# Performance work log

Hardware: AMD Instinct MI355X
Metric: run time of the kernel (lower is better)

## Reference

```python
import jax, jax.numpy as jnp
import numpy as np
import math

H = 8
E = 512
D_K = E // H
NEG = -1000000000.0
# last (and only surviving) row of dist_bar: one threshold per head
DIST_BAR = np.array([0.2, 0.3, 0.4, 0.5, 0.6, 0.7, 0.8, 0.9], dtype=np.float32)


def setup_inputs() -> dict:
    key = jax.random.key(0)
    ks = jax.random.split(key, 12)
    B, N = 8, 1024
    s = 1.0 / math.sqrt(E)
    inp = {
        "query": jax.random.normal(ks[0], (B, N, E), jnp.float32),
        "key": jax.random.normal(ks[1], (B, N, E), jnp.float32),
        "value": jax.random.normal(ks[2], (B, N, E), jnp.float32),
        "dist": jax.random.uniform(ks[3], (B, 1, N, N), jnp.float32),
        "mask": jnp.ones((B, N, N), jnp.int32),
        "Wq": jax.random.normal(ks[4], (E, E), jnp.float32) * s,
        "bq": jnp.zeros((E,), jnp.float32),
        "Wk": jax.random.normal(ks[5], (E, E), jnp.float32) * s,
        "bk": jnp.zeros((E,), jnp.float32),
        "Wv": jax.random.normal(ks[6], (E, E), jnp.float32) * s,
        "bv": jnp.zeros((E,), jnp.float32),
        "Wo": jax.random.normal(ks[7], (E, E), jnp.float32) * s,
        "bo": jnp.zeros((E,), jnp.float32),
    }
    return inp


def reference(query, key, value, dist, mask, Wq, bq, Wk, bk, Wv, bv, Wo, bo):
    B, N, _ = query.shape
    # project and split heads: [B, H, N, D_K]
    def heads(x, W, b):
        return (x @ W.T + b).reshape(B, N, H, D_K).transpose(0, 2, 1, 3)
    q = heads(query, Wq, bq)
    k = heads(key, Wk, bk)
    v = heads(value, Wv, bv)
    scores = jnp.einsum("bhqd,bhkd->bhqk", q, k) / math.sqrt(D_K)
    # padding mask: [B,N,N] -> [B,1,N,N]
    scores = jnp.where(mask[:, None, :, :] == 0, NEG, scores)
    # per-head distance mask: dist [B,1,N,N] < thr[h] -> [B,H,N,N]
    thr = jnp.asarray(DIST_BAR)[None, :, None, None]
    dmask = dist < thr
    # first row/col (global atom) always attend
    dmask = dmask.at[:, :, 0, :].set(True).at[:, :, :, 0].set(True)
    scores = jnp.where(dmask, scores, NEG)
    p = jax.nn.softmax(scores, axis=-1)
    out = jnp.einsum("bhqk,bhkd->bhqd", p, v)  # [B,H,N,D_K]
    out = out.transpose(0, 2, 1, 3).reshape(B, N, H * D_K)
    return out @ Wo.T + bo
```

## Files before the change

### kernel.cpp

```cpp
#include <hip/hip_runtime.h>
#include <stdint.h>


typedef __attribute__((ext_vector_type(8))) short short8;
typedef __attribute__((ext_vector_type(4))) float floatx4;

#define MFMA16(a, b, c) __builtin_amdgcn_mfma_f32_16x16x32_bf16((a), (b), (c), 0, 0, 0)
#define QSCALE 0.1803368801111362f

static __device__ __forceinline__ unsigned short f2bf(float f) {
  union { float f; unsigned u; } v; v.f = f;
  unsigned r = v.u + 0x7fffu + ((v.u >> 16) & 1u);
  return (unsigned short)(r >> 16);
}

static __device__ __forceinline__ void gload_lds16(const void* g, void* l) {
  __builtin_amdgcn_global_load_lds((const __attribute__((address_space(1))) unsigned int*)g,
                                   (__attribute__((address_space(3))) unsigned int*)l,
                                   16, 0, 0);
}
static __device__ __forceinline__ int xsw(int row) { return (row & 3) ^ ((row >> 2) & 3); }

__global__ void cast_all(const float* __restrict__ q, const float* __restrict__ k,
                         const float* __restrict__ v,
                         const float* __restrict__ wq, const float* __restrict__ wk,
                         const float* __restrict__ wv, const float* __restrict__ wo,
                         unsigned short* __restrict__ qb, unsigned short* __restrict__ kb,
                         unsigned short* __restrict__ vb,
                         unsigned short* __restrict__ wq16, unsigned short* __restrict__ wk16,
                         unsigned short* __restrict__ wv16, unsigned short* __restrict__ wo16) {
  int i = blockIdx.x * blockDim.x + threadIdx.x;
  const float* s; unsigned short* d; int loc;
  if (i < 3145728) {
    int w = i >> 20; loc = i & 1048575;
    s = (w == 0) ? q : (w == 1) ? k : v;
    d = (w == 0) ? qb : (w == 1) ? kb : vb;
  } else {
    int j = i - 3145728; int w = j >> 16; loc = j & 65535;
    s = (w == 0) ? wq : (w == 1) ? wk : (w == 2) ? wv : wo;
    d = (w == 0) ? wq16 : (w == 1) ? wk16 : (w == 2) ? wv16 : wo16;
  }
  float4 vv = ((const float4*)s)[loc];
  ushort4 o;
  o.x = f2bf(vv.x); o.y = f2bf(vv.y); o.z = f2bf(vv.z); o.w = f2bf(vv.w);
  ((ushort4*)d)[loc] = o;
}

__global__ void codes_kernel(const float* __restrict__ dist, const int* __restrict__ mask,
                             unsigned char* __restrict__ codesP) {
  int t = blockIdx.x * blockDim.x + threadIdx.x;
  int flat = t << 2;
  int b = flat >> 20;
  int rem = flat & ((1 << 20) - 1);
  int row = rem >> 10;
  int col0 = rem & 1023;
  float4 d4 = ((const float4*)dist)[t];
  int4 m4 = ((const int4*)mask)[t];
  float dv[4] = {d4.x, d4.y, d4.z, d4.w};
  int mv[4] = {m4.x, m4.y, m4.z, m4.w};
  int rg = row >> 5;
  int st = (row >> 4) & 1;
  int qq = (row >> 2) & 3;
  int r = row & 3;
  size_t rowbase = (size_t)(b * 32 + rg) * 32768;
  int sub = st * 32 + r;
#pragma unroll
  for (int u = 0; u < 4; u++) {
    int col = col0 + u;
    float d = dv[u];
    int hmin = (d >= 0.2f) + (d >= 0.3f) + (d >= 0.4f) + (d >= 0.5f) +
               (d >= 0.6f) + (d >= 0.7f) + (d >= 0.8f) + (d >= 0.9f);
    unsigned char cc = (unsigned char)hmin;
    if (row == 0 || col == 0) cc = 0;
    if (mv[u] == 0) cc = 9;
    int kt = col >> 7, ci = (col >> 4) & 7, c = col & 15;
    int lane = qq * 16 + c;
    codesP[rowbase + (size_t)kt * 4096 + lane * 64 + sub + ci * 4] = cc;
  }
}

__global__ __launch_bounds__(256) void qkv_gemm(
    const unsigned short* __restrict__ Aq, const unsigned short* __restrict__ Ak,
    const unsigned short* __restrict__ Av,
    const unsigned short* __restrict__ Wqp, const unsigned short* __restrict__ Wkp,
    const unsigned short* __restrict__ Wvp,
    const float* __restrict__ bq, const float* __restrict__ bk, const float* __restrict__ bv,
    unsigned short* __restrict__ Qh, unsigned short* __restrict__ Kh,
    unsigned short* __restrict__ Vt) {
  const int z = blockIdx.z;
  const unsigned short* A = (z == 0) ? Aq : (z == 1) ? Ak : Av;
  const unsigned short* W = (z == 0) ? Wqp : (z == 1) ? Wkp : Wvp;
  const float* bias = (z == 0) ? bq : (z == 1) ? bk : bv;
  unsigned short* O = (z == 0) ? Qh : (z == 1) ? Kh : Vt;

  __shared__ __align__(16) short As[128 * 32];
  __shared__ __align__(16) short Bs[128 * 32];
  const int tid = threadIdx.x;
  const int lane = tid & 63;
  const int wave = tid >> 6;
  const int c = lane & 15;
  const int q = lane >> 4;
  const int m0 = blockIdx.x * 128;
  const int n0 = blockIdx.y * 128;
  const int wr = (wave >> 1) * 64;
  const int wc = (wave & 1) * 64;

  floatx4 acc[4][4];
#pragma unroll
  for (int i = 0; i < 4; i++)
#pragma unroll
    for (int j = 0; j < 4; j++) acc[i][j] = (floatx4)(0.0f);

  for (int k0 = 0; k0 < 512; k0 += 32) {
    __syncthreads();
#pragma unroll
    for (int it = 0; it < 2; it++) {
      int slot = wave * 128 + it * 64 + lane;
      int row = slot >> 2, ch = slot & 3;
      int g = ch ^ xsw(row);
      gload_lds16(A + (size_t)(m0 + row) * 512 + k0 + g * 8, &As[(wave * 128 + it * 64) * 8]);
      gload_lds16(W + (size_t)(n0 + row) * 512 + k0 + g * 8, &Bs[(wave * 128 + it * 64) * 8]);
    }
    __syncthreads();

    short8 af[4], bfv[4];
#pragma unroll
    for (int i = 0; i < 4; i++) {
      int row = wr + i * 16 + c;
      af[i] = *(const short8*)(&As[row * 32 + (q ^ xsw(row)) * 8]);
    }
#pragma unroll
    for (int j = 0; j < 4; j++) {
      int row = wc + j * 16 + c;
      bfv[j] = *(const short8*)(&Bs[row * 32 + (q ^ xsw(row)) * 8]);
    }
#pragma unroll
    for (int i = 0; i < 4; i++)
#pragma unroll
      for (int j = 0; j < 4; j++)
        acc[i][j] = MFMA16(af[i], bfv[j], acc[i][j]);
  }

  const float scale = (z == 0) ? QSCALE : 1.0f;
#pragma unroll
  for (int i = 0; i < 4; i++) {
    int gm0 = m0 + wr + i * 16 + q * 4;
#pragma unroll
    for (int j = 0; j < 4; j++) {
      int gn = n0 + wc + j * 16 + c;
      float bb = bias[gn];
      int h = gn >> 6, d = gn & 63;
      if (z == 2) {
        int b = gm0 >> 10, n = gm0 & 1023;
        ushort4 pk;
#pragma unroll
        for (int r = 0; r < 4; r++) pk[r] = f2bf(acc[i][j][r] + bb);
        *(ushort4*)(&Vt[(((size_t)(b * 8 + h) * 64 + d) << 10) + n]) = pk;
      } else {
#pragma unroll
        for (int r = 0; r < 4; r++) {
          int m = gm0 + r;
          int b = m >> 10, n = m & 1023;
          O[((((size_t)(b * 8 + h)) << 10) + n) * 64 + d] = f2bf((acc[i][j][r] + bb) * scale);
        }
      }
    }
  }
}

__global__ __launch_bounds__(256) void out_gemm(const unsigned short* __restrict__ A,
                                                const unsigned short* __restrict__ W,
                                                const float* __restrict__ bias,
                                                float* __restrict__ Out) {
  __shared__ __align__(16) short As[128 * 32];
  __shared__ __align__(16) short Bs[64 * 32];
  const int tid = threadIdx.x;
  const int lane = tid & 63;
  const int wave = tid >> 6;
  const int c = lane & 15;
  const int q = lane >> 4;
  const int m0 = blockIdx.x * 128;
  const int n0 = blockIdx.y * 64;
  const int wr = (wave >> 1) * 64;
  const int wc = (wave & 1) * 32;

  floatx4 acc[4][2];
#pragma unroll
  for (int i = 0; i < 4; i++)
#pragma unroll
    for (int j = 0; j < 2; j++) acc[i][j] = (floatx4)(0.0f);

  for (int k0 = 0; k0 < 512; k0 += 32) {
    __syncthreads();
#pragma unroll
    for (int it = 0; it < 2; it++) {
      int slot = wave * 128 + it * 64 + lane;
      int row = slot >> 2, ch = slot & 3;
      int g = ch ^ xsw(row);
      gload_lds16(A + (size_t)(m0 + row) * 512 + k0 + g * 8, &As[(wave * 128 + it * 64) * 8]);
    }
    {
      int slot = wave * 64 + lane;
      int row = slot >> 2, ch = slot & 3;
      int g = ch ^ xsw(row);
      gload_lds16(W + (size_t)(n0 + row) * 512 + k0 + g * 8, &Bs[(wave * 64) * 8]);
    }
    __syncthreads();

    short8 af[4], bfv[2];
#pragma unroll
    for (int i = 0; i < 4; i++) {
      int row = wr + i * 16 + c;
      af[i] = *(const short8*)(&As[row * 32 + (q ^ xsw(row)) * 8]);
    }
#pragma unroll
    for (int j = 0; j < 2; j++) {
      int row = wc + j * 16 + c;
      bfv[j] = *(const short8*)(&Bs[row * 32 + (q ^ xsw(row)) * 8]);
    }
#pragma unroll
    for (int i = 0; i < 4; i++)
#pragma unroll
      for (int j = 0; j < 2; j++)
        acc[i][j] = MFMA16(af[i], bfv[j], acc[i][j]);
  }

#pragma unroll
  for (int i = 0; i < 4; i++) {
    int gm0 = m0 + wr + i * 16 + q * 4;
#pragma unroll
    for (int j = 0; j < 2; j++) {
      int gn = n0 + wc + j * 16 + c;
      float bb = bias[gn];
#pragma unroll
      for (int r = 0; r < 4; r++)
        Out[(size_t)(gm0 + r) * 512 + gn] = acc[i][j][r] + bb;
    }
  }
}

__global__ __launch_bounds__(256) void attn_kernel(const unsigned short* __restrict__ Qh,
                                                   const unsigned short* __restrict__ Kh,
                                                   const unsigned short* __restrict__ Vt,
                                                   const unsigned char* __restrict__ codesP,
                                                   unsigned short* __restrict__ AO) {
  __shared__ __align__(16) unsigned short P[4][16 * 132];
  const int tid = threadIdx.x;
  const int lane = tid & 63;
  const int wave = tid >> 6;
  const int c = lane & 15;
  const int q = lane >> 4;
  const int bh = blockIdx.y;
  const int b = bh >> 3;
  const int h = bh & 7;
  const size_t base = (size_t)bh << 16;
  const int rbase = blockIdx.x * 64 + wave * 16;
  const int rg = rbase >> 5;
  const int st = (rbase >> 4) & 1;
  unsigned short* Pw = &P[wave][0];

  short8 aq[2];
#pragma unroll
  for (int kk = 0; kk < 2; kk++)
    aq[kk] = *(const short8*)(Qh + base + (size_t)(rbase + c) * 64 + kk * 32 + q * 8);

  const unsigned char* cbt = codesP + (size_t)(b * 32 + rg) * 32768 + lane * 64 + st * 32;
  const unsigned short* Kb = Kh + base;
  const unsigned short* Vb = Vt + base;

  float rs[4] = {0.0f, 0.0f, 0.0f, 0.0f};
  floatx4 o[4];
#pragma unroll
  for (int ci = 0; ci < 4; ci++) o[ci] = (floatx4)(0.0f);

  for (int kt = 0; kt < 8; kt++) {
    const unsigned short* Kt = Kb + (size_t)kt * 128 * 64;
    floatx4 s[8];
#pragma unroll
    for (int ci = 0; ci < 8; ci++) s[ci] = (floatx4)(0.0f);
#pragma unroll
    for (int ci = 0; ci < 8; ci++)
#pragma unroll
      for (int kk = 0; kk < 2; kk++) {
        short8 bk = *(const short8*)(Kt + (size_t)(ci * 16 + c) * 64 + kk * 32 + q * 8);
        s[ci] = MFMA16(aq[kk], bk, s[ci]);
      }
    const unsigned char* cp = cbt + (size_t)kt * 4096;
    uint4 w0 = *(const uint4*)(cp);
    uint4 w1 = *(const uint4*)(cp + 16);
    unsigned cv[8] = {w0.x, w0.y, w0.z, w0.w, w1.x, w1.y, w1.z, w1.w};
#pragma unroll
    for (int ci = 0; ci < 8; ci++)
#pragma unroll
      for (int r = 0; r < 4; r++) {
        int code = (cv[ci] >> (r * 8)) & 0xff;
        float e = (h >= code) ? exp2f(s[ci][r]) : 0.0f;
        rs[r] += e;
        Pw[(q * 4 + r) * 132 + ci * 16 + c] = f2bf(e);
      }
#pragma unroll
    for (int ch = 0; ch < 4; ch++) {
      short8 ap = *(const short8*)(&Pw[(size_t)c * 132 + ch * 32 + q * 8]);
#pragma unroll
      for (int ci = 0; ci < 4; ci++) {
        short8 bv = *(const short8*)(Vb + (size_t)(ci * 16 + c) * 1024 + kt * 128 + ch * 32 + q * 8);
        o[ci] = MFMA16(ap, bv, o[ci]);
      }
    }
  }

  float inv[4];
#pragma unroll
  for (int r = 0; r < 4; r++) {
    float v = rs[r];
    v += __shfl_xor(v, 1); v += __shfl_xor(v, 2);
    v += __shfl_xor(v, 4); v += __shfl_xor(v, 8);
    inv[r] = 1.0f / v;
  }
#pragma unroll
  for (int r = 0; r < 4; r++) {
    int n = rbase + q * 4 + r;
    size_t ob = ((size_t)((b << 10) + n)) * 512 + h * 64;
#pragma unroll
    for (int ci = 0; ci < 4; ci++)
      AO[ob + ci * 16 + c] = f2bf(o[ci][r] * inv[r]);
  }
}

extern "C" void kernel_launch(void* const* d_in, const int* in_sizes, int n_in,
                              void* d_out, int out_size, void* d_ws, size_t ws_size,
                              hipStream_t stream) {
  const float* query = (const float*)d_in[0];
  const float* key_  = (const float*)d_in[1];
  const float* value = (const float*)d_in[2];
  const float* dist  = (const float*)d_in[3];
  const int*   mask  = (const int*)d_in[4];
  const float* Wq = (const float*)d_in[5];
  const float* bq = (const float*)d_in[6];
  const float* Wk = (const float*)d_in[7];
  const float* bk = (const float*)d_in[8];
  const float* Wv = (const float*)d_in[9];
  const float* bv = (const float*)d_in[10];
  const float* Wo = (const float*)d_in[11];
  const float* bo = (const float*)d_in[12];

  char* ws = (char*)d_ws;
  size_t off = 0;
  auto alloc = [&](size_t bytes) -> char* {
    char* p = ws + off;
    off += (bytes + 255) & ~(size_t)255;
    return p;
  };
  const size_t NQKV = 8192ull * 512;
  unsigned short* qb   = (unsigned short*)alloc(NQKV * 2);
  unsigned short* kb   = (unsigned short*)alloc(NQKV * 2);
  unsigned short* vb   = (unsigned short*)alloc(NQKV * 2);
  unsigned short* wq16 = (unsigned short*)alloc(512ull * 512 * 2);
  unsigned short* wk16 = (unsigned short*)alloc(512ull * 512 * 2);
  unsigned short* wv16 = (unsigned short*)alloc(512ull * 512 * 2);
  unsigned short* wo16 = (unsigned short*)alloc(512ull * 512 * 2);
  unsigned short* Qh = (unsigned short*)alloc(NQKV * 2);
  unsigned short* Kh = (unsigned short*)alloc(NQKV * 2);
  unsigned short* Vt = (unsigned short*)alloc(NQKV * 2);
  unsigned short* AO = (unsigned short*)alloc(NQKV * 2);
  unsigned char*  codesP = (unsigned char*)alloc(8ull * 1024 * 1024);

  cast_all<<<13312, 256, 0, stream>>>(query, key_, value, Wq, Wk, Wv, Wo,
                                      qb, kb, vb, wq16, wk16, wv16, wo16);
  codes_kernel<<<8192, 256, 0, stream>>>(dist, mask, codesP);
  qkv_gemm<<<dim3(64, 4, 3), 256, 0, stream>>>(qb, kb, vb, wq16, wk16, wv16,
                                               bq, bk, bv, Qh, Kh, Vt);
  attn_kernel<<<dim3(16, 64), 256, 0, stream>>>(Qh, Kh, Vt, codesP, AO);
  out_gemm<<<dim3(64, 8), 256, 0, stream>>>(AO, wo16, bo, (float*)d_out);
}
```

Before: 332.8 us.

## Split KV across wave pairs in attention, merge prep kernels, vectorize QK stores

The attention kernel now has each wave handle 32 query rows (two 16-row subtiles) over half of the key range. This reuses each K and V fragment load for two MFMAs, and partial outputs and row sums are combined through LDS after a block barrier. The cast and codes kernels are merged into one launch. The Q/K projection epilogue swaps operand roles so results can be written as packed ushort4 stores instead of scalar ones. In exchange, register pressure, LDS use and an extra synchronization step go up.

```diff
diff --git a/kernel.cpp b/kernel.cpp
--- a/kernel.cpp
+++ b/kernel.cpp
@@ -21,80 +21,82 @@
 }
 static __device__ __forceinline__ int xsw(int row) { return (row & 3) ^ ((row >> 2) & 3); }
 
-__global__ void cast_all(const float* __restrict__ q, const float* __restrict__ k,
-                         const float* __restrict__ v,
-                         const float* __restrict__ wq, const float* __restrict__ wk,
-                         const float* __restrict__ wv, const float* __restrict__ wo,
-                         unsigned short* __restrict__ qb, unsigned short* __restrict__ kb,
-                         unsigned short* __restrict__ vb,
-                         unsigned short* __restrict__ wq16, unsigned short* __restrict__ wk16,
-                         unsigned short* __restrict__ wv16, unsigned short* __restrict__ wo16) {
-  int i = blockIdx.x * blockDim.x + threadIdx.x;
-  const float* s; unsigned short* d; int loc;
-  if (i < 3145728) {
-    int w = i >> 20; loc = i & 1048575;
-    s = (w == 0) ? q : (w == 1) ? k : v;
-    d = (w == 0) ? qb : (w == 1) ? kb : vb;
+__global__ void prep_kernel(const float* __restrict__ q, const float* __restrict__ k,
+                            const float* __restrict__ v,
+                            const float* __restrict__ wq, const float* __restrict__ wk,
+                            const float* __restrict__ wv, const float* __restrict__ wo,
+                            const float* __restrict__ dist, const int* __restrict__ mask,
+                            unsigned short* __restrict__ qb, unsigned short* __restrict__ kb,
+                            unsigned short* __restrict__ vb,
+                            unsigned short* __restrict__ wq16, unsigned short* __restrict__ wk16,
+                            unsigned short* __restrict__ wv16, unsigned short* __restrict__ wo16,
+                            unsigned char* __restrict__ codesP) {
+  int gb = blockIdx.x;
+  if (gb < 13312) {
+    int i = gb * 256 + threadIdx.x;
+    const float* s; unsigned short* d; int loc;
+    if (i < 3145728) {
+      int w = i >> 20; loc = i & 1048575;
+      s = (w == 0) ? q : (w == 1) ? k : v;
+      d = (w == 0) ? qb : (w == 1) ? kb : vb;
+    } else {
+      int j = i - 3145728; int w = j >> 16; loc = j & 65535;
+      s = (w == 0) ? wq : (w == 1) ? wk : (w == 2) ? wv : wo;
+      d = (w == 0) ? wq16 : (w == 1) ? wk16 : (w == 2) ? wv16 : wo16;
+    }
+    float4 vv = ((const float4*)s)[loc];
+    ushort4 o;
+    o.x = f2bf(vv.x); o.y = f2bf(vv.y); o.z = f2bf(vv.z); o.w = f2bf(vv.w);
+    ((ushort4*)d)[loc] = o;
   } else {
-    int j = i - 3145728; int w = j >> 16; loc = j & 65535;
-    s = (w == 0) ? wq : (w == 1) ? wk : (w == 2) ? wv : wo;
-    d = (w == 0) ? wq16 : (w == 1) ? wk16 : (w == 2) ? wv16 : wo16;
-  }
-  float4 vv = ((const float4*)s)[loc];
-  ushort4 o;
-  o.x = f2bf(vv.x); o.y = f2bf(vv.y); o.z = f2bf(vv.z); o.w = f2bf(vv.w);
-  ((ushort4*)d)[loc] = o;
-}
-
-__global__ void codes_kernel(const float* __restrict__ dist, const int* __restrict__ mask,
-                             unsigned char* __restrict__ codesP) {
-  int t = blockIdx.x * blockDim.x + threadIdx.x;
-  int flat = t << 2;
-  int b = flat >> 20;
-  int rem = flat & ((1 << 20) - 1);
-  int row = rem >> 10;
-  int col0 = rem & 1023;
-  float4 d4 = ((const float4*)dist)[t];
-  int4 m4 = ((const int4*)mask)[t];
-  float dv[4] = {d4.x, d4.y, d4.z, d4.w};
-  int mv[4] = {m4.x, m4.y, m4.z, m4.w};
-  int rg = row >> 5;
-  int st = (row >> 4) & 1;
-  int qq = (row >> 2) & 3;
-  int r = row & 3;
-  size_t rowbase = (size_t)(b * 32 + rg) * 32768;
-  int sub = st * 32 + r;
-#pragma unroll
-  for (int u = 0; u < 4; u++) {
-    int col = col0 + u;
-    float d = dv[u];
-    int hmin = (d >= 0.2f) + (d >= 0.3f) + (d >= 0.4f) + (d >= 0.5f) +
-               (d >= 0.6f) + (d >= 0.7f) + (d >= 0.8f) + (d >= 0.9f);
-    unsigned char cc = (unsigned char)hmin;
-    if (row == 0 || col == 0) cc = 0;
-    if (mv[u] == 0) cc = 9;
-    int kt = col >> 7, ci = (col >> 4) & 7, c = col & 15;
-    int lane = qq * 16 + c;
-    codesP[rowbase + (size_t)kt * 4096 + lane * 64 + sub + ci * 4] = cc;
+    int t = (gb - 13312) * 256 + threadIdx.x;
+    int flat = t << 2;
+    int b = flat >> 20;
+    int rem = flat & ((1 << 20) - 1);
+    int row = rem >> 10;
+    int col0 = rem & 1023;
+    float4 d4 = ((const float4*)dist)[t];
+    int4 m4 = ((const int4*)mask)[t];
+    float dv[4] = {d4.x, d4.y, d4.z, d4.w};
+    int mv[4] = {m4.x, m4.y, m4.z, m4.w};
+    int rg = row >> 5;
+    int st = (row >> 4) & 1;
+    int qq = (row >> 2) & 3;
+    int r = row & 3;
+    size_t rowbase = (size_t)(b * 32 + rg) * 32768;
+    int sub = st * 32 + r;
+#pragma unroll
+    for (int u = 0; u < 4; u++) {
+      int col = col0 + u;
+      float d = dv[u];
+      int hmin = (d >= 0.2f) + (d >= 0.3f) + (d >= 0.4f) + (d >= 0.5f) +
+                 (d >= 0.6f) + (d >= 0.7f) + (d >= 0.8f) + (d >= 0.9f);
+      unsigned char cc = (unsigned char)hmin;
+      if (row == 0 || col == 0) cc = 0;
+      if (mv[u] == 0) cc = 9;
+      int kt = col >> 7, ci = (col >> 4) & 7, c = col & 15;
+      int lane = qq * 16 + c;
+      codesP[rowbase + (size_t)kt * 4096 + lane * 64 + sub + ci * 4] = cc;
+    }
   }
 }
 
 __global__ __launch_bounds__(256) void qkv_gemm(
-    const unsigned short* __restrict__ Aq, const unsigned short* __restrict__ Ak,
-    const unsigned short* __restrict__ Av,
+    const unsigned short* __restrict__ Xq, const unsigned short* __restrict__ Xk,
+    const unsigned short* __restrict__ Xv,
     const unsigned short* __restrict__ Wqp, const unsigned short* __restrict__ Wkp,
     const unsigned short* __restrict__ Wvp,
     const float* __restrict__ bq, const float* __restrict__ bk, const float* __restrict__ bv,
     unsigned short* __restrict__ Qh, unsigned short* __restrict__ Kh,
     unsigned short* __restrict__ Vt) {
   const int z = blockIdx.z;
-  const unsigned short* A = (z == 0) ? Aq : (z == 1) ? Ak : Av;
+  const unsigned short* X = (z == 0) ? Xq : (z == 1) ? Xk : Xv;
   const unsigned short* W = (z == 0) ? Wqp : (z == 1) ? Wkp : Wvp;
   const float* bias = (z == 0) ? bq : (z == 1) ? bk : bv;
   unsigned short* O = (z == 0) ? Qh : (z == 1) ? Kh : Vt;
 
-  __shared__ __align__(16) short As[128 * 32];
-  __shared__ __align__(16) short Bs[128 * 32];
+  __shared__ __align__(16) short Xs[128 * 32];
+  __shared__ __align__(16) short Ws[128 * 32];
   const int tid = threadIdx.x;
   const int lane = tid & 63;
   const int wave = tid >> 6;
@@ -118,21 +120,23 @@
       int slot = wave * 128 + it * 64 + lane;
       int row = slot >> 2, ch = slot & 3;
       int g = ch ^ xsw(row);
-      gload_lds16(A + (size_t)(m0 + row) * 512 + k0 + g * 8, &As[(wave * 128 + it * 64) * 8]);
-      gload_lds16(W + (size_t)(n0 + row) * 512 + k0 + g * 8, &Bs[(wave * 128 + it * 64) * 8]);
+      gload_lds16(X + (size_t)(m0 + row) * 512 + k0 + g * 8, &Xs[(wave * 128 + it * 64) * 8]);
+      gload_lds16(W + (size_t)(n0 + row) * 512 + k0 + g * 8, &Ws[(wave * 128 + it * 64) * 8]);
     }
     __syncthreads();
 
+    const short* Pa = (z == 2) ? Xs : Ws;
+    const short* Pb = (z == 2) ? Ws : Xs;
     short8 af[4], bfv[4];
 #pragma unroll
     for (int i = 0; i < 4; i++) {
       int row = wr + i * 16 + c;
-      af[i] = *(const short8*)(&As[row * 32 + (q ^ xsw(row)) * 8]);
+      af[i] = *(const short8*)(&Pa[row * 32 + (q ^ xsw(row)) * 8]);
     }
 #pragma unroll
     for (int j = 0; j < 4; j++) {
       int row = wc + j * 16 + c;
-      bfv[j] = *(const short8*)(&Bs[row * 32 + (q ^ xsw(row)) * 8]);
+      bfv[j] = *(const short8*)(&Pb[row * 32 + (q ^ xsw(row)) * 8]);
     }
 #pragma unroll
     for (int i = 0; i < 4; i++)
@@ -141,28 +145,38 @@
         acc[i][j] = MFMA16(af[i], bfv[j], acc[i][j]);
   }
 
-  const float scale = (z == 0) ? QSCALE : 1.0f;
-#pragma unroll
-  for (int i = 0; i < 4; i++) {
-    int gm0 = m0 + wr + i * 16 + q * 4;
-#pragma unroll
-    for (int j = 0; j < 4; j++) {
-      int gn = n0 + wc + j * 16 + c;
-      float bb = bias[gn];
-      int h = gn >> 6, d = gn & 63;
-      if (z == 2) {
-        int b = gm0 >> 10, n = gm0 & 1023;
+  if (z == 2) {
+#pragma unroll
+    for (int i = 0; i < 4; i++) {
+      int gm0 = m0 + wr + i * 16 + q * 4;
+      int b = gm0 >> 10, n = gm0 & 1023;
+#pragma unroll
+      for (int j = 0; j < 4; j++) {
+        int gn = n0 + wc + j * 16 + c;
+        float bb = bias[gn];
+        int h = gn >> 6, d = gn & 63;
         ushort4 pk;
 #pragma unroll
         for (int r = 0; r < 4; r++) pk[r] = f2bf(acc[i][j][r] + bb);
         *(ushort4*)(&Vt[(((size_t)(b * 8 + h) * 64 + d) << 10) + n]) = pk;
-      } else {
-#pragma unroll
-        for (int r = 0; r < 4; r++) {
-          int m = gm0 + r;
-          int b = m >> 10, n = m & 1023;
-          O[((((size_t)(b * 8 + h)) << 10) + n) * 64 + d] = f2bf((acc[i][j][r] + bb) * scale);
-        }
+      }
+    }
+  } else {
+    const float scale = (z == 0) ? QSCALE : 1.0f;
+#pragma unroll
+    for (int i = 0; i < 4; i++) {
+      int f0 = n0 + wr + i * 16 + q * 4;
+      float4 bb4 = *(const float4*)(bias + f0);
+      int h = f0 >> 6, d0 = f0 & 63;
+      float bbs[4] = {bb4.x, bb4.y, bb4.z, bb4.w};
+#pragma unroll
+      for (int j = 0; j < 4; j++) {
+        int t = m0 + wc + j * 16 + c;
+        int b = t >> 10, n = t & 1023;
+        ushort4 pk;
+#pragma unroll
+        for (int r = 0; r < 4; r++) pk[r] = f2bf((acc[i][j][r] + bbs[r]) * scale);
+        *(ushort4*)(&O[((((size_t)(b * 8 + h)) << 10) + n) * 64 + d0]) = pk;
       }
     }
   }
@@ -239,12 +253,13 @@
   }
 }
 
-__global__ __launch_bounds__(256) void attn_kernel(const unsigned short* __restrict__ Qh,
-                                                   const unsigned short* __restrict__ Kh,
-                                                   const unsigned short* __restrict__ Vt,
-                                                   const unsigned char* __restrict__ codesP,
-                                                   unsigned short* __restrict__ AO) {
-  __shared__ __align__(16) unsigned short P[4][16 * 132];
+__global__ __launch_bounds__(256, 4) void attn_kernel(const unsigned short* __restrict__ Qh,
+                                                      const unsigned short* __restrict__ Kh,
+                                                      const unsigned short* __restrict__ Vt,
+                                                      const unsigned char* __restrict__ codesP,
+                                                      unsigned short* __restrict__ AO) {
+  __shared__ __align__(16) unsigned short P[4][32 * 132];
+  __shared__ float rsx[2][32];
   const int tid = threadIdx.x;
   const int lane = tid & 63;
   const int wave = tid >> 6;
@@ -254,76 +269,126 @@
   const int b = bh >> 3;
   const int h = bh & 7;
   const size_t base = (size_t)bh << 16;
-  const int rbase = blockIdx.x * 64 + wave * 16;
+  const int qc = wave >> 1;
+  const int kvh = wave & 1;
+  const int rbase = blockIdx.x * 64 + qc * 32;
   const int rg = rbase >> 5;
-  const int st = (rbase >> 4) & 1;
   unsigned short* Pw = &P[wave][0];
 
-  short8 aq[2];
-#pragma unroll
-  for (int kk = 0; kk < 2; kk++)
-    aq[kk] = *(const short8*)(Qh + base + (size_t)(rbase + c) * 64 + kk * 32 + q * 8);
-
-  const unsigned char* cbt = codesP + (size_t)(b * 32 + rg) * 32768 + lane * 64 + st * 32;
+  short8 aq[2][2];
+#pragma unroll
+  for (int st = 0; st < 2; st++)
+#pragma unroll
+    for (int kk = 0; kk < 2; kk++)
+      aq[st][kk] = *(const short8*)(Qh + base + (size_t)(rbase + st * 16 + c) * 64 + kk * 32 + q * 8);
+
+  const unsigned char* cbt = codesP + (size_t)(b * 32 + rg) * 32768 + lane * 64;
   const unsigned short* Kb = Kh + base;
   const unsigned short* Vb = Vt + base;
 
-  float rs[4] = {0.0f, 0.0f, 0.0f, 0.0f};
-  floatx4 o[4];
-#pragma unroll
-  for (int ci = 0; ci < 4; ci++) o[ci] = (floatx4)(0.0f);
-
-  for (int kt = 0; kt < 8; kt++) {
+  float rs[2][4];
+#pragma unroll
+  for (int st = 0; st < 2; st++)
+#pragma unroll
+    for (int r = 0; r < 4; r++) rs[st][r] = 0.0f;
+  floatx4 o[2][4];
+#pragma unroll
+  for (int st = 0; st < 2; st++)
+#pragma unroll
+    for (int ci = 0; ci < 4; ci++) o[st][ci] = (floatx4)(0.0f);
+
+  for (int kt = kvh * 4; kt < kvh * 4 + 4; kt++) {
     const unsigned short* Kt = Kb + (size_t)kt * 128 * 64;
-    floatx4 s[8];
-#pragma unroll
-    for (int ci = 0; ci < 8; ci++) s[ci] = (floatx4)(0.0f);
+    floatx4 s[2][8];
+#pragma unroll
+    for (int ci = 0; ci < 8; ci++) { s[0][ci] = (floatx4)(0.0f); s[1][ci] = (floatx4)(0.0f); }
 #pragma unroll
     for (int ci = 0; ci < 8; ci++)
 #pragma unroll
       for (int kk = 0; kk < 2; kk++) {
         short8 bk = *(const short8*)(Kt + (size_t)(ci * 16 + c) * 64 + kk * 32 + q * 8);
-        s[ci] = MFMA16(aq[kk], bk, s[ci]);
+        s[0][ci] = MFMA16(aq[0][kk], bk, s[0][ci]);
+        s[1][ci] = MFMA16(aq[1][kk], bk, s[1][ci]);
       }
     const unsigned char* cp = cbt + (size_t)kt * 4096;
     uint4 w0 = *(const uint4*)(cp);
     uint4 w1 = *(const uint4*)(cp + 16);
-    unsigned cv[8] = {w0.x, w0.y, w0.z, w0.w, w1.x, w1.y, w1.z, w1.w};
-#pragma unroll
-    for (int ci = 0; ci < 8; ci++)
-#pragma unroll
-      for (int r = 0; r < 4; r++) {
-        int code = (cv[ci] >> (r * 8)) & 0xff;
-        float e = (h >= code) ? exp2f(s[ci][r]) : 0.0f;
-        rs[r] += e;
-        Pw[(q * 4 + r) * 132 + ci * 16 + c] = f2bf(e);
-      }
+    uint4 w2 = *(const uint4*)(cp + 32);
+    uint4 w3 = *(const uint4*)(cp + 48);
+    unsigned cv[16] = {w0.x, w0.y, w0.z, w0.w, w1.x, w1.y, w1.z, w1.w,
+                       w2.x, w2.y, w2.z, w2.w, w3.x, w3.y, w3.z, w3.w};
+#pragma unroll
+    for (int st = 0; st < 2; st++)
+#pragma unroll
+      for (int ci = 0; ci < 8; ci++)
+#pragma unroll
+        for (int r = 0; r < 4; r++) {
+          int bidx = st * 32 + ci * 4 + r;
+          int code = (cv[bidx >> 2] >> ((bidx & 3) * 8)) & 0xff;
+          float e = (h >= code) ? exp2f(s[st][ci][r]) : 0.0f;
+          rs[st][r] += e;
+          Pw[(st * 16 + q * 4 + r) * 132 + ci * 16 + c] = f2bf(e);
+        }
 #pragma unroll
     for (int ch = 0; ch < 4; ch++) {
-      short8 ap = *(const short8*)(&Pw[(size_t)c * 132 + ch * 32 + q * 8]);
+      short8 ap0 = *(const short8*)(&Pw[(size_t)c * 132 + ch * 32 + q * 8]);
+      short8 ap1 = *(const short8*)(&Pw[(size_t)(16 + c) * 132 + ch * 32 + q * 8]);
 #pragma unroll
       for (int ci = 0; ci < 4; ci++) {
         short8 bv = *(const short8*)(Vb + (size_t)(ci * 16 + c) * 1024 + kt * 128 + ch * 32 + q * 8);
-        o[ci] = MFMA16(ap, bv, o[ci]);
+        o[0][ci] = MFMA16(ap0, bv, o[0][ci]);
+        o[1][ci] = MFMA16(ap1, bv, o[1][ci]);
       }
     }
   }
 
-  float inv[4];
-#pragma unroll
-  for (int r = 0; r < 4; r++) {
-    float v = rs[r];
-    v += __shfl_xor(v, 1); v += __shfl_xor(v, 2);
-    v += __shfl_xor(v, 4); v += __shfl_xor(v, 8);
-    inv[r] = 1.0f / v;
-  }
-#pragma unroll
-  for (int r = 0; r < 4; r++) {
-    int n = rbase + q * 4 + r;
-    size_t ob = ((size_t)((b << 10) + n)) * 512 + h * 64;
-#pragma unroll
-    for (int ci = 0; ci < 4; ci++)
-      AO[ob + ci * 16 + c] = f2bf(o[ci][r] * inv[r]);
+#pragma unroll
+  for (int st = 0; st < 2; st++)
+#pragma unroll
+    for (int r = 0; r < 4; r++) {
+      float v = rs[st][r];
+      v += __shfl_xor(v, 1); v += __shfl_xor(v, 2);
+      v += __shfl_xor(v, 4); v += __shfl_xor(v, 8);
+      rs[st][r] = v;
+    }
+
+  float* dump = (float*)&P[qc * 2 + 1][0];
+  if (kvh == 1) {
+#pragma unroll
+    for (int st = 0; st < 2; st++)
+#pragma unroll
+      for (int ci = 0; ci < 4; ci++)
+        *(floatx4*)(dump + lane * 32 + (st * 4 + ci) * 4) = o[st][ci];
+    if (c == 0) {
+#pragma unroll
+      for (int st = 0; st < 2; st++)
+#pragma unroll
+        for (int r = 0; r < 4; r++) rsx[qc][st * 16 + q * 4 + r] = rs[st][r];
+    }
+  }
+  __syncthreads();
+  if (kvh == 0) {
+    float inv[2][4];
+#pragma unroll
+    for (int st = 0; st < 2; st++)
+#pragma unroll
+      for (int ci = 0; ci < 4; ci++)
+        o[st][ci] += *(const floatx4*)(dump + lane * 32 + (st * 4 + ci) * 4);
+#pragma unroll
+    for (int st = 0; st < 2; st++)
+#pragma unroll
+      for (int r = 0; r < 4; r++)
+        inv[st][r] = 1.0f / (rs[st][r] + rsx[qc][st * 16 + q * 4 + r]);
+#pragma unroll
+    for (int st = 0; st < 2; st++)
+#pragma unroll
+      for (int r = 0; r < 4; r++) {
+        int n = rbase + st * 16 + q * 4 + r;
+        size_t ob = ((size_t)((b << 10) + n)) * 512 + h * 64;
+#pragma unroll
+        for (int ci = 0; ci < 4; ci++)
+          AO[ob + ci * 16 + c] = f2bf(o[st][ci][r] * inv[st][r]);
+      }
   }
 }
 
@@ -365,9 +430,8 @@
   unsigned short* AO = (unsigned short*)alloc(NQKV * 2);
   unsigned char*  codesP = (unsigned char*)alloc(8ull * 1024 * 1024);
 
-  cast_all<<<13312, 256, 0, stream>>>(query, key_, value, Wq, Wk, Wv, Wo,
-                                      qb, kb, vb, wq16, wk16, wv16, wo16);
-  codes_kernel<<<8192, 256, 0, stream>>>(dist, mask, codesP);
+  prep_kernel<<<21504, 256, 0, stream>>>(query, key_, value, Wq, Wk, Wv, Wo, dist, mask,
+                                         qb, kb, vb, wq16, wk16, wv16, wo16, codesP);
   qkv_gemm<<<dim3(64, 4, 3), 256, 0, stream>>>(qb, kb, vb, wq16, wk16, wv16,
                                                bq, bk, bv, Qh, Kh, Vt);
   attn_kernel<<<dim3(16, 64), 256, 0, stream>>>(Qh, Kh, Vt, codesP, AO);
```

Measured after the change: 296.5 us. 1.12x faster.
